# Kernel tuning notes

Hardware: AMD Instinct MI355X
Metric: run time of the kernel (lower is better)

Reference implementation:

```python
import jax, jax.numpy as jnp
import numpy as np

E = 512      # moe_experts
M = 6        # per-expert dim = moe_dim // 2
H = 6        # moe_heads
D = 1024     # hidden_size
F = E * M    # flatten_shape = 3072

def relu2(x):
    return jnp.square(jax.nn.relu(x))

def setup_inputs() -> dict:
    key = jax.random.key(0)
    ks = jax.random.split(key, 12)
    B, S = 4, 2048
    inp = {
        "x": jax.random.normal(ks[0], (B, S, D), jnp.float32),
        "g1": jax.random.uniform(ks[1], (B, S, H, E), jnp.float32),
        "g2": jax.random.uniform(ks[2], (B, S, H, E), jnp.float32),
        "u1_w": jax.random.normal(ks[3], (F, D), jnp.float32) * 0.02,
        "u1_b": jnp.zeros((F,), jnp.float32),
        "u2_w": jax.random.normal(ks[4], (F, D), jnp.float32) * 0.02,
        "u2_b": jnp.zeros((F,), jnp.float32),
        "v11_w": jax.random.normal(ks[5], (D // 2, F), jnp.float32) * 0.02,
        "v12_w": jax.random.normal(ks[6], (D // 2, F), jnp.float32) * 0.02,
        "v21_w": jax.random.normal(ks[7], (D // 2, F), jnp.float32) * 0.02,
        "v22_w": jax.random.normal(ks[8], (D // 2, F), jnp.float32) * 0.02,
        "b1": jnp.zeros((E, D // 2), jnp.float32),
        "b2": jnp.zeros((E, D // 2), jnp.float32),
    }
    return inp

def reference(x, g1, g2, u1_w, u1_b, u2_w, u2_b, v11_w, v12_w, v21_w, v22_w, b1, b2):
    B, S, _ = x.shape
    # up-proj + relu^2, split into (experts E, per-expert dim M)
    x1 = relu2(x @ u1_w.T + u1_b).reshape(B, S, E, M)   # [B,S,E,M]
    x2 = relu2(x @ u2_w.T + u2_b).reshape(B, S, E, M)
    # gate sums over heads
    gs1 = jnp.einsum('bshi,bsim->bsim', g1, x1)          # sum_h g1 applied to x1
    gs2 = jnp.einsum('bshj,bsjm->bsjm', g2, x2)
    x11 = gs1.reshape(B, S, F) @ v11_w.T                 # [B,S,D/2]
    x22 = gs2.reshape(B, S, F) @ v22_w.T
    # cross terms: contract over h efficiently (avoid E x E materialization)
    t2 = jnp.einsum('bshj,bsjm->bshm', g2, x2)           # [B,S,H,M]
    x12 = jnp.einsum('bshm,bshi->bsim', t2, g1).reshape(B, S, F) @ v12_w.T
    t1 = jnp.einsum('bshi,bsim->bshm', g1, x1)
    x21 = jnp.einsum('bshm,bshj->bsjm', t1, g2).reshape(B, S, F) @ v21_w.T
    # bias terms through gates
    x13 = jnp.einsum('bshi,id->bsd', g1, b1)
    x23 = jnp.einsum('bshj,jd->bsd', g2, b2)
    return jnp.concatenate((x11 + x12 + x13, x21 + x22 + x23), axis=-1)
```

## Files before the change

kernel.cpp:

```cpp
#include <hip/hip_runtime.h>
#include <stdint.h>

typedef unsigned short u16;
typedef unsigned int u32;
typedef __attribute__((ext_vector_type(8))) short bf16x8;
typedef __attribute__((ext_vector_type(4))) float f32x4;

__device__ __forceinline__ float bf2f(u16 u) {
    unsigned v = ((unsigned)u) << 16;
    float f;
    __builtin_memcpy(&f, &v, 4);
    return f;
}
__device__ __forceinline__ u16 f2bf(float f) {
    unsigned x;
    __builtin_memcpy(&x, &f, 4);
    unsigned r = (x + 0x7fffu + ((x >> 16) & 1u)) >> 16;
    return (u16)r;
}

#define GLDS(g, l) __builtin_amdgcn_global_load_lds( \
    (const __attribute__((address_space(1))) void*)(g), \
    (__attribute__((address_space(3))) void*)(l), 16, 0, 0)

#define BARX() do { asm volatile("" ::: "memory"); __builtin_amdgcn_s_barrier(); asm volatile("" ::: "memory"); } while (0)
#define LGKM0() asm volatile("s_waitcnt lgkmcnt(0)" ::: "memory")
#define WAIT_VM4() asm volatile("s_waitcnt vmcnt(4)" ::: "memory")
#define WAIT_VM0() asm volatile("s_waitcnt vmcnt(0)" ::: "memory")

__device__ __forceinline__ void gemm256_core(
    const u16* gA, const u16* gB, size_t ldk, int NT,
    u16* lds, int tid, f32x4 (&acc)[8][4])
{
    const int lane  = tid & 63;
    const int wave  = tid >> 6;
    const int wr    = wave >> 2;
    const int wc    = wave & 3;
    const int mlane = lane & 15;
    const int quad  = lane >> 4;
    const int swz   = mlane & 7;

    u16* A0 = lds;
    u16* B0 = lds + 16384;
    u16* A1 = lds + 32768;
    u16* B1 = lds + 49152;

    #define ST_A(h, t, dst) do { \
        GLDS(gA + (size_t)((h)*128     ) * ldk + (size_t)(t) * 64, (dst) + (h)*8192 + tid*8); \
        GLDS(gA + (size_t)((h)*128 + 64) * ldk + (size_t)(t) * 64, (dst) + (h)*8192 + 4096 + tid*8); \
    } while (0)
    #define ST_B(h, t, dst) do { \
        GLDS(gB + (size_t)((h)*128     ) * ldk + (size_t)(t) * 64, (dst) + (h)*8192 + tid*8); \
        GLDS(gB + (size_t)((h)*128 + 64) * ldk + (size_t)(t) * 64, (dst) + (h)*8192 + 4096 + tid*8); \
    } while (0)
    #define RD_A(dst, buf, mh, kh) do { \
        _Pragma("unroll") \
        for (int m = 0; m < 4; ++m) { \
            const int r = wr*128 + ((mh)*4 + m)*16 + mlane; \
            dst[m] = *(const bf16x8*)((buf) + r*64 + ((((kh)*4 + quad) ^ swz) * 8)); \
        } \
    } while (0)
    #define RD_B(dst, buf, nh, kh) do { \
        _Pragma("unroll") \
        for (int n = 0; n < 2; ++n) { \
            const int r = wc*64 + ((nh)*2 + n)*16 + mlane; \
            dst[n] = *(const bf16x8*)((buf) + r*64 + ((((kh)*4 + quad) ^ swz) * 8)); \
        } \
    } while (0)
    #define MM8(aS, bS, MB, NB) do { \
        __builtin_amdgcn_s_setprio(1); \
        _Pragma("unroll") \
        for (int m = 0; m < 4; ++m) \
            _Pragma("unroll") \
            for (int n = 0; n < 2; ++n) \
                acc[(MB) + m][(NB) + n] = __builtin_amdgcn_mfma_f32_16x16x32_bf16( \
                    aS[m], bS[n], acc[(MB) + m][(NB) + n], 0, 0, 0); \
        __builtin_amdgcn_s_setprio(0); \
    } while (0)

    ST_A(0, 0, A0); ST_A(1, 0, A0);
    ST_B(0, 0, B0); ST_B(1, 0, B0);
    ST_B(0, 1, B1); ST_B(1, 1, B1);
    WAIT_VM4();
    BARX();

    bf16x8 a0[4], a1[4], b0[2], b1[2];
    RD_A(a0, A0, 0, 0);
    RD_B(b0, B0, 0, 0);

    for (int u = 0; u < NT; ++u) {
        u16* bA = (u & 1) ? A1 : A0;
        u16* bB = (u & 1) ? B1 : B0;
        u16* oA = (u & 1) ? A0 : A1;
        u16* nB = (u & 1) ? B0 : B1;

        RD_A(a1, bA, 1, 0);
        MM8(a0, b0, 0, 0);
        RD_B(b1, bB, 1, 0);
        MM8(a1, b0, 4, 0);
        MM8(a1, b1, 4, 2);
        RD_A(a1, bA, 0, 1);
        RD_B(b0, bB, 1, 1);
        MM8(a0, b1, 0, 2);
        RD_A(a0, bA, 1, 1);
        if (u + 1 < NT) { ST_A(0, u + 1, oA); ST_A(1, u + 1, oA); }
        MM8(a1, b0, 0, 2);
        RD_B(b1, bB, 0, 1);
        MM8(a0, b0, 4, 2);
        LGKM0();
        BARX();
        if (u + 2 < NT) ST_B(0, u + 2, bB);
        MM8(a0, b1, 4, 0);
        if (u + 2 < NT) ST_B(1, u + 2, bB);
        MM8(a1, b1, 0, 0);

        if (u + 1 < NT) {
            if (u + 2 < NT) { WAIT_VM4(); } else { WAIT_VM0(); }
            BARX();
            RD_A(a0, oA, 0, 0);
            RD_B(b0, nB, 0, 0);
        }
    }
    #undef ST_A
    #undef ST_B
    #undef RD_A
    #undef RD_B
    #undef MM8
}

__global__ __launch_bounds__(512, 2) void gemm1_8ph(
    const u16* __restrict__ X, const u16* __restrict__ U1, const u16* __restrict__ U2,
    const float* __restrict__ bias1, const float* __restrict__ bias2,
    u16* __restrict__ Y1, u16* __restrict__ Y2)
{
    __shared__ __align__(16) u16 lds[65536];
    const int tid = threadIdx.x;
    const int z = blockIdx.z;
    const int rowBase = blockIdx.y * 256;
    const int colBase = blockIdx.x * 256;
    const int r0 = tid >> 3;
    const int cs = ((tid & 7) ^ (r0 & 7)) * 8;
    const u16* gA = X + (size_t)(rowBase + r0) * 1024 + cs;
    const u16* gB = (z ? U2 : U1) + (size_t)(colBase + r0) * 1024 + cs;

    f32x4 acc[8][4] = {};
    gemm256_core(gA, gB, 1024, 16, lds, tid, acc);

    const float* bias = z ? bias2 : bias1;
    u16* outp = z ? Y2 : Y1;
    const int coloff = z * 3072;
    const int lane = tid & 63, wave = tid >> 6;
    const int wr = wave >> 2, wc = wave & 3;
    const int mlane = lane & 15, quad = lane >> 4;
    #pragma unroll
    for (int n = 0; n < 4; ++n) {
        const int col = colBase + wc * 64 + n * 16 + mlane;
        const float bv = bias[col];
        #pragma unroll
        for (int m = 0; m < 8; ++m) {
            const int rb = rowBase + wr * 128 + m * 16 + quad * 4;
            #pragma unroll
            for (int r = 0; r < 4; ++r) {
                float v = acc[m][n][r] + bv;
                v = (v > 0.0f) ? v * v : 0.0f;
                outp[(size_t)(rb + r) * 6656 + coloff + col] = f2bf(v);
            }
        }
    }
}

__global__ __launch_bounds__(512, 2) void gemm2_8ph(
    const u16* __restrict__ Y1, const u16* __restrict__ Y2,
    const u16* __restrict__ W1, const u16* __restrict__ W2,
    float* __restrict__ out, float* __restrict__ part, int nsplit)
{
    __shared__ __align__(16) u16 lds[65536];
    const int tid = threadIdx.x;
    const int z2 = blockIdx.z;
    const int z = z2 & 1;
    const int split = z2 >> 1;
    const int Ks = 6656 / nsplit;
    const int kbeg = split * Ks;
    const int rowBase = blockIdx.y * 256;
    const int colBase = blockIdx.x * 256;
    const int r0 = tid >> 3;
    const int cs = ((tid & 7) ^ (r0 & 7)) * 8;
    const u16* gA = (z ? Y2 : Y1) + (size_t)(rowBase + r0) * 6656 + kbeg + cs;
    const u16* gB = (z ? W2 : W1) + (size_t)(colBase + r0) * 6656 + kbeg + cs;

    f32x4 acc[8][4] = {};
    gemm256_core(gA, gB, 6656, Ks >> 6, lds, tid, acc);

    float* dst = split ? part : out;
    const int coloff = z * 512;
    const int lane = tid & 63, wave = tid >> 6;
    const int wr = wave >> 2, wc = wave & 3;
    const int mlane = lane & 15, quad = lane >> 4;
    #pragma unroll
    for (int n = 0; n < 4; ++n) {
        const int col = colBase + wc * 64 + n * 16 + mlane;
        #pragma unroll
        for (int m = 0; m < 8; ++m) {
            const int rb = rowBase + wr * 128 + m * 16 + quad * 4;
            #pragma unroll
            for (int r = 0; r < 4; ++r)
                dst[(size_t)(rb + r) * 1024 + coloff + col] = acc[m][n][r];
        }
    }
}

__global__ __launch_bounds__(256) void reduce_add(
    float4* __restrict__ out, const float4* __restrict__ p, int nadd)
{
    const int i = blockIdx.x * 256 + threadIdx.x;
    float4 v = out[i];
    for (int k = 0; k < nadd; ++k) {
        const float4 a = p[(size_t)k * 2097152 + i];
        v.x += a.x; v.y += a.y; v.z += a.z; v.w += a.w;
    }
    out[i] = v;
}

__global__ __launch_bounds__(256) void cvt_bf16(
    const float* __restrict__ x, const float* __restrict__ u1,
    const float* __restrict__ u2, u16* __restrict__ dst)
{
    const int idx4 = blockIdx.x * 256 + threadIdx.x;
    const int NX = 8388608 / 4, NU = 3145728 / 4;
    const float4* src;
    int off;
    if (idx4 < NX)           { src = (const float4*)x;  off = idx4; }
    else if (idx4 < NX + NU) { src = (const float4*)u1; off = idx4 - NX; }
    else                     { src = (const float4*)u2; off = idx4 - NX - NU; }
    const float4 v = src[off];
    ushort4 o;
    o.x = f2bf(v.x); o.y = f2bf(v.y); o.z = f2bf(v.z); o.w = f2bf(v.w);
    ((ushort4*)dst)[idx4] = o;
}

__global__ __launch_bounds__(256) void prep_wcat(
    const float* __restrict__ v11, const float* __restrict__ v12,
    const float* __restrict__ v21, const float* __restrict__ v22,
    const float* __restrict__ b1,  const float* __restrict__ b2,
    u16* __restrict__ W1, u16* __restrict__ W2)
{
    const int idx = blockIdx.x * 256 + threadIdx.x;
    const int n = idx / 6656;
    const int k = idx - n * 6656;
    float w1, w2;
    if (k < 3072)      { w1 = v11[n * 3072 + k];        w2 = v21[n * 3072 + k]; }
    else if (k < 6144) { w1 = v12[n * 3072 + k - 3072]; w2 = v22[n * 3072 + k - 3072]; }
    else               { w1 = b1[(k - 6144) * 512 + n]; w2 = b2[(k - 6144) * 512 + n]; }
    W1[idx] = f2bf(w1);
    W2[idx] = f2bf(w2);
}

__global__ __launch_bounds__(256) void gating(
    const float* __restrict__ g1, const float* __restrict__ g2,
    u16* __restrict__ Y1, u16* __restrict__ Y2)
{
    __shared__ __align__(16) u16 sm[17408];
    __shared__ float tls[72];
    u16* g1b = sm;
    u16* xT1 = sm + 3072;
    u16* g2b = sm + 6144;
    u16* xT2 = sm + 9216;
    const int tid = threadIdx.x;
    const int wave = tid >> 6, lane = tid & 63;
    const size_t tok = blockIdx.x;
    const size_t gb = tok * 3072;
    const size_t yb = tok * 6656;

    #pragma unroll
    for (int j = 0; j < 3; ++j) {
        const int c = tid + j * 256;
        float4 a = ((const float4*)(g1 + gb))[c];
        float4 bq = ((const float4*)(g2 + gb))[c];
        ushort4 oa, ob;
        oa.x = f2bf(a.x); oa.y = f2bf(a.y); oa.z = f2bf(a.z); oa.w = f2bf(a.w);
        ob.x = f2bf(bq.x); ob.y = f2bf(bq.y); ob.z = f2bf(bq.z); ob.w = f2bf(bq.w);
        ((ushort4*)g1b)[c] = oa;
        ((ushort4*)g2b)[c] = ob;
        ushort4 xv1 = ((const ushort4*)(Y1 + yb))[c];
        ushort4 xv2 = ((const ushort4*)(Y2 + yb + 3072))[c];
        const u16 v1[4] = {xv1.x, xv1.y, xv1.z, xv1.w};
        const u16 v2[4] = {xv2.x, xv2.y, xv2.z, xv2.w};
        #pragma unroll
        for (int q = 0; q < 4; ++q) {
            const int e = c * 4 + q;
            const int i = e / 6;
            const int m = e - 6 * i;
            xT1[m * 512 + i] = v1[q];
            xT2[m * 512 + i] = v2[q];
        }
    }
    __syncthreads();

    if (wave < 2) {
        const u16* Ab = wave ? g2b : g1b;
        const u16* Bb = wave ? xT2 : xT1;
        const int fofs = (lane & 15) * 512 + (lane >> 4) * 8;
        f32x4 acc = {};
        #pragma unroll
        for (int k0 = 0; k0 < 512; k0 += 32) {
            bf16x8 af = *(const bf16x8*)(Ab + fofs + k0);
            bf16x8 bf = *(const bf16x8*)(Bb + fofs + k0);
            acc = __builtin_amdgcn_mfma_f32_16x16x32_bf16(af, bf, acc, 0, 0, 0);
        }
        const int col = lane & 15;
        const int rowb = (lane >> 4) * 4;
        float* ts = tls + wave * 36;
        #pragma unroll
        for (int r = 0; r < 4; ++r) {
            const int row = rowb + r;
            if (row < 6 && col < 6) ts[row * 6 + col] = acc[r];
        }
    }
    __syncthreads();

    const int t = tid;
    u32* Y1d = (u32*)(Y1 + yb);
    u32* Y2d = (u32*)(Y2 + yb);
    float sp1[2], sp2[2];
    #pragma unroll
    for (int e = 0; e < 2; ++e) {
        const int i = 2 * t + e;
        float g1v[6], g2v[6];
        float s1 = 0.f, s2 = 0.f;
        #pragma unroll
        for (int h = 0; h < 6; ++h) {
            g1v[h] = bf2f(g1b[h * 512 + i]); s1 += g1v[h];
            g2v[h] = bf2f(g2b[h * 512 + i]); s2 += g2v[h];
        }
        sp1[e] = s1; sp2[e] = s2;
        u32 pa1[3], pc2[3], pc1[3], pa2[3];
        #pragma unroll
        for (int mq = 0; mq < 3; ++mq) {
            u32 wa1 = 0, wc2 = 0, wc1 = 0, wa2 = 0;
            #pragma unroll
            for (int half = 0; half < 2; ++half) {
                const int m = mq * 2 + half;
                const float x1 = bf2f(xT1[m * 512 + i]);
                const float x2 = bf2f(xT2[m * 512 + i]);
                const float a1 = s1 * x1;
                const float a2 = s2 * x2;
                float c1 = 0.f, c2 = 0.f;
                #pragma unroll
                for (int h = 0; h < 6; ++h) {
                    c2 += tls[36 + h * 6 + m] * g1v[h];
                    c1 += tls[h * 6 + m] * g2v[h];
                }
                const int sh = half * 16;
                wa1 |= ((u32)f2bf(a1)) << sh;
                wc2 |= ((u32)f2bf(c2)) << sh;
                wc1 |= ((u32)f2bf(c1)) << sh;
                wa2 |= ((u32)f2bf(a2)) << sh;
            }
            pa1[mq] = wa1; pc2[mq] = wc2; pc1[mq] = wc1; pa2[mq] = wa2;
        }
        const int base = 6 * t + 3 * e;
        #pragma unroll
        for (int mq = 0; mq < 3; ++mq) {
            Y1d[base + mq]        = pa1[mq];
            Y1d[1536 + base + mq] = pc2[mq];
            Y2d[base + mq]        = pc1[mq];
            Y2d[1536 + base + mq] = pa2[mq];
        }
    }
    Y1d[3072 + t] = (u32)f2bf(sp1[0]) | (((u32)f2bf(sp1[1])) << 16);
    Y2d[3072 + t] = (u32)f2bf(sp2[0]) | (((u32)f2bf(sp2[1])) << 16);
}

extern "C" void kernel_launch(void* const* d_in, const int* in_sizes, int n_in,
                              void* d_out, int out_size, void* d_ws, size_t ws_size,
                              hipStream_t stream) {
    const float* x   = (const float*)d_in[0];
    const float* g1  = (const float*)d_in[1];
    const float* g2  = (const float*)d_in[2];
    const float* u1w = (const float*)d_in[3];
    const float* u1b = (const float*)d_in[4];
    const float* u2w = (const float*)d_in[5];
    const float* u2b = (const float*)d_in[6];
    const float* v11 = (const float*)d_in[7];
    const float* v12 = (const float*)d_in[8];
    const float* v21 = (const float*)d_in[9];
    const float* v22 = (const float*)d_in[10];
    const float* b1  = (const float*)d_in[11];
    const float* b2  = (const float*)d_in[12];
    float* out = (float*)d_out;

    u16* Y1   = (u16*)d_ws;
    u16* Y2   = Y1 + (size_t)8192 * 6656;
    u16* xbf  = Y2 + (size_t)8192 * 6656;
    u16* u1bf = xbf + (size_t)8192 * 1024;
    u16* u2bf = u1bf + (size_t)3072 * 1024;
    u16* W1   = u2bf + (size_t)3072 * 1024;
    u16* W2   = W1 + (size_t)512 * 6656;
    float* part = (float*)(W2 + (size_t)512 * 6656);

    const size_t base = (size_t)(W2 + (size_t)512 * 6656 - (u16*)d_ws) * 2;
    const size_t pbytes = (size_t)8192 * 1024 * 4;
    const int nsplit = (ws_size >= base + pbytes) ? 2 : 1;

    cvt_bf16<<<dim3(14336), 256, 0, stream>>>(x, u1w, u2w, xbf);
    prep_wcat<<<dim3(13312), 256, 0, stream>>>(v11, v12, v21, v22, b1, b2, W1, W2);

    gemm1_8ph<<<dim3(12, 32, 2), 512, 0, stream>>>(
        xbf, u1bf, u2bf, u1b, u2b, Y1, Y2);

    gating<<<dim3(8192), 256, 0, stream>>>(g1, g2, Y1, Y2);

    gemm2_8ph<<<dim3(2, 32, 2 * nsplit), 512, 0, stream>>>(
        Y1, Y2, W1, W2, out, part, nsplit);
    if (nsplit > 1)
        reduce_add<<<dim3(8192), 256, 0, stream>>>(
            (float4*)out, (const float4*)part, nsplit - 1);
}
```

Baseline: 586.0 us.

## Restructure GEMM main loop into barrier-separated quadrant phases and add XCD-aware block swizzle

Replaces the interleaved register-ping-pong GEMM loop with a schedule of four phases per K-tile. Each phase loads a full K-slice of A/B fragments from LDS and is separated from its MFMA quadrant by workgroup barriers. Global-to-LDS prefetch now runs two tiles ahead for both A and B, with a deeper vmcnt wait. The 3D grids become 1D and are remapped so neighbouring tiles land on the same XCD, aiming at better L2 reuse. The added barriers and larger fragment register arrays could reduce overlap or occupancy.

```diff
diff --git a/kernel.cpp b/kernel.cpp
--- a/kernel.cpp
+++ b/kernel.cpp
@@ -24,8 +24,7 @@
     (__attribute__((address_space(3))) void*)(l), 16, 0, 0)
 
 #define BARX() do { asm volatile("" ::: "memory"); __builtin_amdgcn_s_barrier(); asm volatile("" ::: "memory"); } while (0)
-#define LGKM0() asm volatile("s_waitcnt lgkmcnt(0)" ::: "memory")
-#define WAIT_VM4() asm volatile("s_waitcnt vmcnt(4)" ::: "memory")
+#define WAIT_VM8() asm volatile("s_waitcnt vmcnt(8)" ::: "memory")
 #define WAIT_VM0() asm volatile("s_waitcnt vmcnt(0)" ::: "memory")
 
 __device__ __forceinline__ void gemm256_core(
@@ -53,79 +52,84 @@
         GLDS(gB + (size_t)((h)*128     ) * ldk + (size_t)(t) * 64, (dst) + (h)*8192 + tid*8); \
         GLDS(gB + (size_t)((h)*128 + 64) * ldk + (size_t)(t) * 64, (dst) + (h)*8192 + 4096 + tid*8); \
     } while (0)
-    #define RD_A(dst, buf, mh, kh) do { \
+    #define RD_A(buf, mh) do { \
         _Pragma("unroll") \
         for (int m = 0; m < 4; ++m) { \
             const int r = wr*128 + ((mh)*4 + m)*16 + mlane; \
-            dst[m] = *(const bf16x8*)((buf) + r*64 + ((((kh)*4 + quad) ^ swz) * 8)); \
+            _Pragma("unroll") \
+            for (int kk = 0; kk < 2; ++kk) \
+                a[m][kk] = *(const bf16x8*)((buf) + r*64 + (((kk*4 + quad) ^ swz) * 8)); \
         } \
     } while (0)
-    #define RD_B(dst, buf, nh, kh) do { \
+    #define RD_B(buf, nh) do { \
         _Pragma("unroll") \
         for (int n = 0; n < 2; ++n) { \
             const int r = wc*64 + ((nh)*2 + n)*16 + mlane; \
-            dst[n] = *(const bf16x8*)((buf) + r*64 + ((((kh)*4 + quad) ^ swz) * 8)); \
+            _Pragma("unroll") \
+            for (int kk = 0; kk < 2; ++kk) \
+                b[(nh)*2 + n][kk] = *(const bf16x8*)((buf) + r*64 + (((kk*4 + quad) ^ swz) * 8)); \
         } \
     } while (0)
-    #define MM8(aS, bS, MB, NB) do { \
+    #define MFMA_Q(MB, NB) do { \
         __builtin_amdgcn_s_setprio(1); \
         _Pragma("unroll") \
         for (int m = 0; m < 4; ++m) \
             _Pragma("unroll") \
             for (int n = 0; n < 2; ++n) \
-                acc[(MB) + m][(NB) + n] = __builtin_amdgcn_mfma_f32_16x16x32_bf16( \
-                    aS[m], bS[n], acc[(MB) + m][(NB) + n], 0, 0, 0); \
+                _Pragma("unroll") \
+                for (int kk = 0; kk < 2; ++kk) \
+                    acc[(MB) + m][(NB) + n] = __builtin_amdgcn_mfma_f32_16x16x32_bf16( \
+                        a[m][kk], b[(NB) + n][kk], acc[(MB) + m][(NB) + n], 0, 0, 0); \
         __builtin_amdgcn_s_setprio(0); \
     } while (0)
 
-    ST_A(0, 0, A0); ST_A(1, 0, A0);
-    ST_B(0, 0, B0); ST_B(1, 0, B0);
-    ST_B(0, 1, B1); ST_B(1, 1, B1);
-    WAIT_VM4();
+    ST_A(0, 0, A0); ST_B(0, 0, B0); ST_A(1, 0, A0); ST_B(1, 0, B0);
+    if (NT > 1) {
+        ST_A(0, 1, A1); ST_B(0, 1, B1); ST_A(1, 1, A1); ST_B(1, 1, B1);
+        WAIT_VM8();
+    } else {
+        WAIT_VM0();
+    }
     BARX();
 
-    bf16x8 a0[4], a1[4], b0[2], b1[2];
-    RD_A(a0, A0, 0, 0);
-    RD_B(b0, B0, 0, 0);
+    bf16x8 a[4][2], b[4][2];
 
     for (int u = 0; u < NT; ++u) {
         u16* bA = (u & 1) ? A1 : A0;
         u16* bB = (u & 1) ? B1 : B0;
-        u16* oA = (u & 1) ? A0 : A1;
-        u16* nB = (u & 1) ? B0 : B1;
-
-        RD_A(a1, bA, 1, 0);
-        MM8(a0, b0, 0, 0);
-        RD_B(b1, bB, 1, 0);
-        MM8(a1, b0, 4, 0);
-        MM8(a1, b1, 4, 2);
-        RD_A(a1, bA, 0, 1);
-        RD_B(b0, bB, 1, 1);
-        MM8(a0, b1, 0, 2);
-        RD_A(a0, bA, 1, 1);
-        if (u + 1 < NT) { ST_A(0, u + 1, oA); ST_A(1, u + 1, oA); }
-        MM8(a1, b0, 0, 2);
-        RD_B(b1, bB, 0, 1);
-        MM8(a0, b0, 4, 2);
-        LGKM0();
-        BARX();
-        if (u + 2 < NT) ST_B(0, u + 2, bB);
-        MM8(a0, b1, 4, 0);
-        if (u + 2 < NT) ST_B(1, u + 2, bB);
-        MM8(a1, b1, 0, 0);
-
-        if (u + 1 < NT) {
-            if (u + 2 < NT) { WAIT_VM4(); } else { WAIT_VM0(); }
-            BARX();
-            RD_A(a0, oA, 0, 0);
-            RD_B(b0, nB, 0, 0);
-        }
+
+        RD_A(bA, 0);
+        RD_B(bB, 0);
+        BARX();
+        MFMA_Q(0, 0);
+        BARX();
+
+        RD_B(bB, 1);
+        BARX();
+        MFMA_Q(0, 2);
+        BARX();
+
+        RD_A(bA, 1);
+        if (u + 2 < NT) { ST_B(0, u + 2, bB); ST_B(1, u + 2, bB); }
+        BARX();
+        MFMA_Q(4, 2);
+        BARX();
+
+        if (u + 2 < NT) { ST_A(0, u + 2, bA); ST_A(1, u + 2, bA); }
+        BARX();
+        MFMA_Q(4, 0);
+        if (u + 2 < NT) { WAIT_VM8(); } else if (u + 1 < NT) { WAIT_VM0(); }
+        BARX();
     }
     #undef ST_A
     #undef ST_B
     #undef RD_A
     #undef RD_B
-    #undef MM8
+    #undef MFMA_Q
+}
+
+__device__ __forceinline__ int xcd_swz(int orig, int nwg) {
+    return (orig & 7) * (nwg >> 3) + (orig >> 3);
 }
 
 __global__ __launch_bounds__(512, 2) void gemm1_8ph(
@@ -135,9 +139,12 @@
 {
     __shared__ __align__(16) u16 lds[65536];
     const int tid = threadIdx.x;
-    const int z = blockIdx.z;
-    const int rowBase = blockIdx.y * 256;
-    const int colBase = blockIdx.x * 256;
+    const int w = xcd_swz(blockIdx.x, 768);
+    const int bx = w % 12;
+    const int by = (w / 12) % 32;
+    const int z  = w / (12 * 32);
+    const int rowBase = by * 256;
+    const int colBase = bx * 256;
     const int r0 = tid >> 3;
     const int cs = ((tid & 7) ^ (r0 & 7)) * 8;
     const u16* gA = X + (size_t)(rowBase + r0) * 1024 + cs;
@@ -176,13 +183,16 @@
 {
     __shared__ __align__(16) u16 lds[65536];
     const int tid = threadIdx.x;
-    const int z2 = blockIdx.z;
+    const int w = xcd_swz(blockIdx.x, 128 * nsplit);
+    const int bx = w % 2;
+    const int by = (w / 2) % 32;
+    const int z2 = w / 64;
     const int z = z2 & 1;
     const int split = z2 >> 1;
     const int Ks = 6656 / nsplit;
     const int kbeg = split * Ks;
-    const int rowBase = blockIdx.y * 256;
-    const int colBase = blockIdx.x * 256;
+    const int rowBase = by * 256;
+    const int colBase = bx * 256;
     const int r0 = tid >> 3;
     const int cs = ((tid & 7) ^ (r0 & 7)) * 8;
     const u16* gA = (z ? Y2 : Y1) + (size_t)(rowBase + r0) * 6656 + kbeg + cs;
@@ -405,12 +415,12 @@
     cvt_bf16<<<dim3(14336), 256, 0, stream>>>(x, u1w, u2w, xbf);
     prep_wcat<<<dim3(13312), 256, 0, stream>>>(v11, v12, v21, v22, b1, b2, W1, W2);
 
-    gemm1_8ph<<<dim3(12, 32, 2), 512, 0, stream>>>(
+    gemm1_8ph<<<dim3(768), 512, 0, stream>>>(
         xbf, u1bf, u2bf, u1b, u2b, Y1, Y2);
 
     gating<<<dim3(8192), 256, 0, stream>>>(g1, g2, Y1, Y2);
 
-    gemm2_8ph<<<dim3(2, 32, 2 * nsplit), 512, 0, stream>>>(
+    gemm2_8ph<<<dim3(128 * nsplit), 512, 0, stream>>>(
         Y1, Y2, W1, W2, out, part, nsplit);
     if (nsplit > 1)
         reduce_add<<<dim3(8192), 256, 0, stream>>>(
```

Result: slower. 604.7 us (+3.2%).
